# Performance work log

Measured on AMD Instinct MI355X. Metric: run time of the kernel, lower is better.

## Reference

```python
import jax, jax.numpy as jnp
import numpy as np

B, S, D = 4, 2048, 1024
H = 8  # hardcoded in AttentionLayer
HD = D // H
FF = 4096
EPS = 1e-5


def _layernorm(x):
    # LayerNorm(hidden_dim, elementwise_affine=False), eps=1e-5
    mu = jnp.mean(x, axis=-1, keepdims=True)
    var = jnp.var(x, axis=-1, keepdims=True)
    return (x - mu) / jnp.sqrt(var + EPS)


def setup_inputs() -> dict:
    key = jax.random.key(0)
    ks = jax.random.split(key, 5)
    scale = 0.02
    return {
        "x": jax.random.normal(ks[0], (B, S, D), dtype=jnp.float32),
        "qkv_proj": jax.random.normal(ks[1], (D, 3 * D), dtype=jnp.float32) * scale,
        "o_proj": jax.random.normal(ks[2], (D, D), dtype=jnp.float32) * scale,
        "ff1": jax.random.normal(ks[3], (D, FF), dtype=jnp.float32) * scale,
        "ff2": jax.random.normal(ks[4], (FF, D), dtype=jnp.float32) * scale,
    }


def reference(x, qkv_proj, o_proj, ff1, ff2):
    b, s, d = x.shape
    # --- attention ---
    qkv = jnp.matmul(x, qkv_proj)                       # [b,s,3d]
    qkv = qkv.reshape(b, s, H, 3 * HD).transpose(0, 2, 1, 3)  # [b,h,s,3hd]
    q, k, v = jnp.split(qkv, 3, axis=-1)                # each [b,h,s,hd]
    logits = jnp.einsum('bhqd,bhkd->bhqk', q, k) / jnp.sqrt(jnp.float32(HD))
    attn = jax.nn.softmax(logits, axis=-1)
    vals = jnp.einsum('bhqk,bhkd->bhqd', attn, v)       # [b,h,s,hd]
    vals = vals.transpose(0, 2, 1, 3).reshape(b, s, d)
    attn_out = jnp.matmul(vals, o_proj)
    # --- residual + norm + FFN + residual + norm ---
    x = _layernorm(x + attn_out)
    ff_out = jnp.matmul(jax.nn.relu(jnp.matmul(x, ff1)), ff2)
    x = _layernorm(x + ff_out)
    return x
```

## Files before the change

kernel.cpp:

```cpp
#include <hip/hip_runtime.h>
#include <hip/hip_bf16.h>


typedef float floatx4 __attribute__((ext_vector_type(4)));
typedef float floatx16 __attribute__((ext_vector_type(16)));
typedef short bf16x8 __attribute__((ext_vector_type(8)));

#define DEVI __device__ __forceinline__

typedef const __attribute__((address_space(1))) unsigned int* gas1_t;
typedef __attribute__((address_space(3))) unsigned int* las3_t;

DEVI void gll16(const void* g, void* l) {
  __builtin_amdgcn_global_load_lds((gas1_t)g, (las3_t)l, 16, 0, 0);
}

DEVI short bfbits(float f) {
  __hip_bfloat16 h = __float2bfloat16(f);
  return *reinterpret_cast<short*>(&h);
}

template<int EPI>
__global__ __launch_bounds__(256) void gemm_bt(
    const __hip_bfloat16* __restrict__ A,
    const __hip_bfloat16* __restrict__ BT,
    float* __restrict__ Cf, __hip_bfloat16* __restrict__ Cb,
    const float* __restrict__ Rf, const __hip_bfloat16* __restrict__ Rb,
    int M, int N, int K)
{
  __shared__ __hip_bfloat16 As[128 * 32];
  __shared__ __hip_bfloat16 Bs[128 * 32];
  const int tid = threadIdx.x;
  const int wave = tid >> 6, lane = tid & 63;
  const int lane15 = lane & 15, quad = lane >> 4;
  const int row0 = blockIdx.x * 128, col0 = blockIdx.y * 128;
  const int wr = (wave >> 1) * 64, wc = (wave & 1) * 64;

  floatx4 acc[4][4] = {};

  const int swg = ((tid & 3) ^ ((tid >> 2) & 3)) * 8;
  const __hip_bfloat16* Ag = A + (size_t)(row0 + (tid >> 2)) * K + swg;
  const __hip_bfloat16* Bg = BT + (size_t)(col0 + (tid >> 2)) * K + swg;
  char* Asl = (char*)As + tid * 16;
  char* Bsl = (char*)Bs + tid * 16;
  const size_t rstep = (size_t)64 * K;

  for (int k0 = 0; k0 < K; k0 += 32) {
    __syncthreads();
    gll16(Ag + k0, Asl);
    gll16(Ag + k0 + rstep, Asl + 4096);
    gll16(Bg + k0, Bsl);
    gll16(Bg + k0 + rstep, Bsl + 4096);
    __syncthreads();
    bf16x8 af[4], bb[4];
#pragma unroll
    for (int t = 0; t < 4; t++) {
      const int r = wr + t * 16 + lane15;
      af[t] = *(const bf16x8*)((const char*)As + (size_t)(r * 4 + (quad ^ (lane15 & 3))) * 16);
    }
#pragma unroll
    for (int t = 0; t < 4; t++) {
      const int r = wc + t * 16 + lane15;
      bb[t] = *(const bf16x8*)((const char*)Bs + (size_t)(r * 4 + (quad ^ (lane15 & 3))) * 16);
    }
#pragma unroll
    for (int i = 0; i < 4; i++)
#pragma unroll
      for (int j = 0; j < 4; j++)
        acc[i][j] = __builtin_amdgcn_mfma_f32_16x16x32_bf16(af[i], bb[j], acc[i][j], 0, 0, 0);
  }

#pragma unroll
  for (int i = 0; i < 4; i++) {
    const int mb = row0 + wr + i * 16 + quad * 4;
#pragma unroll
    for (int j = 0; j < 4; j++) {
      const int n = col0 + wc + j * 16 + lane15;
#pragma unroll
      for (int r = 0; r < 4; r++) {
        const size_t idx = (size_t)(mb + r) * N + n;
        const float v = acc[i][j][r];
        if (EPI == 0) {
          Cb[idx] = __float2bfloat16(v);
        } else if (EPI == 1) {
          Cf[idx] = v + Rf[idx];
        } else if (EPI == 2) {
          Cb[idx] = __float2bfloat16(v > 0.f ? v : 0.f);
        } else {
          Cf[idx] = v + __bfloat162float(Rb[idx]);
        }
      }
    }
  }
}

__global__ __launch_bounds__(256, 2) void attn_kernel(
    const __hip_bfloat16* __restrict__ qkv,
    const __hip_bfloat16* __restrict__ Vt,
    __hip_bfloat16* __restrict__ vals)
{
  __shared__ __hip_bfloat16 KVs[128 * 128];
  __shared__ __hip_bfloat16 QP[128 * 128];

  const int tid = threadIdx.x;
  const int wave = tid >> 6, lane = tid & 63;
  const int l31 = lane & 31, l5 = lane >> 5;
  const int qt = blockIdx.x, bh = blockIdx.y;
  const int b = bh >> 3, h = bh & 7;
  const size_t tokbase = (size_t)b * 2048;
  const float scale = 0.08838834764831845f;

  const int sw8 = ((tid & 15) ^ (tid >> 4)) * 8;
  const int srow = tid >> 4;
  const __hip_bfloat16* qg  = qkv + (tokbase + qt * 128) * 3072 + h * 384 + sw8;
  const __hip_bfloat16* kg0 = qkv + tokbase * 3072 + h * 384 + 128 + sw8;
  const __hip_bfloat16* vg0 = Vt + (size_t)bh * 128 * 2048 + sw8;

#pragma unroll
  for (int rd = 0; rd < 8; rd++)
    gll16(qg + (size_t)(rd * 16 + srow) * 3072, (char*)QP + rd * 4096 + tid * 16);
  __syncthreads();

  const int rx = l31 & 15;
  bf16x8 qf[8];
  {
    const char* qb = (const char*)QP + (wave * 32 + l31) * 256;
#pragma unroll
    for (int ks = 0; ks < 8; ks++)
      qf[ks] = *(const bf16x8*)(qb + (((ks * 2 + l5) ^ rx) << 4));
  }

  floatx16 oacc[4] = {};
  float lsum[16];
#pragma unroll
  for (int r = 0; r < 16; r++) lsum[r] = 0.f;

  for (int kt = 0; kt < 16; kt++) {
    __syncthreads();
#pragma unroll
    for (int rd = 0; rd < 8; rd++)
      gll16(kg0 + (size_t)(kt * 128 + rd * 16 + srow) * 3072,
            (char*)KVs + rd * 4096 + tid * 16);
    __syncthreads();

    floatx16 sacc[4] = {};
#pragma unroll
    for (int ks = 0; ks < 8; ks++) {
      const char* kb = (const char*)KVs + l31 * 256 + (((ks * 2 + l5) ^ rx) << 4);
#pragma unroll
      for (int nt = 0; nt < 4; nt++) {
        const bf16x8 bk = *(const bf16x8*)(kb + nt * 8192);
        sacc[nt] = __builtin_amdgcn_mfma_f32_32x32x16_bf16(qf[ks], bk, sacc[nt], 0, 0, 0);
      }
    }

    const int pbase = wave * 8192 + l5 * 1024 + (l31 & 7) * 2;
#pragma unroll
    for (int g = 0; g < 4; g++) {
      const int hgx = l5 + 2 * (g & 1);
#pragma unroll
      for (int r3 = 0; r3 < 4; r3++) {
        const int r = g * 4 + r3;
        const int rowoff = (r3 << 8) + (g << 11) + ((((l31 >> 3) ^ r3)) << 4);
        float part = 0.f;
#pragma unroll
        for (int t = 0; t < 4; t++) {
          const float p = __expf(sacc[t][r] * scale);
          part += p;
          *(short*)((char*)QP + pbase + rowoff + ((t ^ hgx) << 6)) = bfbits(p);
        }
        lsum[r] += part;
      }
    }

    __syncthreads();
#pragma unroll
    for (int rd = 0; rd < 8; rd++)
      gll16(vg0 + (size_t)kt * 128 + (size_t)(rd * 16 + srow) * 2048,
            (char*)KVs + rd * 4096 + tid * 16);
    __syncthreads();

#pragma unroll
    for (int ks = 0; ks < 8; ks++) {
      const bf16x8 ap = *(const bf16x8*)((const char*)QP +
          (wave * 32 + l31) * 256 + (((ks * 2 + l5) ^ rx) << 4));
      const char* vb = (const char*)KVs + l31 * 256 + (((ks * 2 + l5) ^ rx) << 4);
#pragma unroll
      for (int nt = 0; nt < 4; nt++) {
        const bf16x8 bv = *(const bf16x8*)(vb + nt * 8192);
        oacc[nt] = __builtin_amdgcn_mfma_f32_32x32x16_bf16(ap, bv, oacc[nt], 0, 0, 0);
      }
    }
  }

#pragma unroll
  for (int r = 0; r < 16; r++) {
#pragma unroll
    for (int off = 1; off < 32; off <<= 1)
      lsum[r] += __shfl_xor(lsum[r], off);
  }

  const size_t orow0 = tokbase + (size_t)qt * 128 + wave * 32;
#pragma unroll
  for (int g = 0; g < 4; g++) {
#pragma unroll
    for (int r3 = 0; r3 < 4; r3++) {
      const int r = g * 4 + r3;
      const float linv = 1.f / lsum[r];
      const size_t row = orow0 + r3 + 8 * g + 4 * l5;
#pragma unroll
      for (int nt = 0; nt < 4; nt++)
        vals[row * 1024 + h * 128 + nt * 32 + l31] =
            __float2bfloat16(oacc[nt][r] * linv);
    }
  }
}

__global__ __launch_bounds__(256) void cvt_bf16_k(const float* __restrict__ in,
                                                  __hip_bfloat16* __restrict__ out) {
  const size_t i = (size_t)blockIdx.x * 256 + threadIdx.x;
  const float4 v = ((const float4*)in)[i];
  short4 sv;
  sv.x = bfbits(v.x); sv.y = bfbits(v.y); sv.z = bfbits(v.z); sv.w = bfbits(v.w);
  ((short4*)out)[i] = sv;
}

__global__ __launch_bounds__(256) void wtrans_k(const float* __restrict__ W,
                                                __hip_bfloat16* __restrict__ WT,
                                                int K, int N) {
  __shared__ float t[32][33];
  const int tx = threadIdx.x & 31, ty = threadIdx.x >> 5;
  const int n0 = blockIdx.x * 32, k0 = blockIdx.y * 32;
#pragma unroll
  for (int i = 0; i < 4; i++)
    t[ty + i * 8][tx] = W[(size_t)(k0 + ty + i * 8) * N + n0 + tx];
  __syncthreads();
#pragma unroll
  for (int i = 0; i < 4; i++)
    WT[(size_t)(n0 + ty + i * 8) * K + k0 + tx] = __float2bfloat16(t[tx][ty + i * 8]);
}

__global__ __launch_bounds__(256) void vtrans_k(const __hip_bfloat16* __restrict__ qkv,
                                                __hip_bfloat16* __restrict__ Vt) {
  __shared__ __hip_bfloat16 t[32][33];
  const int tx = threadIdx.x & 31, ty = threadIdx.x >> 5;
  const int s0 = blockIdx.x * 32, d0 = blockIdx.y * 32, bh = blockIdx.z;
  const int b = bh >> 3, h = bh & 7;
#pragma unroll
  for (int i = 0; i < 4; i++)
    t[ty + i * 8][tx] = qkv[((size_t)b * 2048 + s0 + ty + i * 8) * 3072 + h * 384 + 256 + d0 + tx];
  __syncthreads();
#pragma unroll
  for (int i = 0; i < 4; i++)
    Vt[((size_t)bh * 128 + d0 + ty + i * 8) * 2048 + s0 + tx] = t[tx][ty + i * 8];
}

template<bool FINAL>
__global__ __launch_bounds__(256) void ln_k(const float* __restrict__ y,
                                            __hip_bfloat16* __restrict__ ob,
                                            float* __restrict__ of) {
  const int row = blockIdx.x, tid = threadIdx.x;
  const float4 v = ((const float4*)(y + (size_t)row * 1024))[tid];
  float s = v.x + v.y + v.z + v.w;
  float q = v.x * v.x + v.y * v.y + v.z * v.z + v.w * v.w;
#pragma unroll
  for (int off = 32; off; off >>= 1) { s += __shfl_xor(s, off); q += __shfl_xor(q, off); }
  __shared__ float ss[4], sq[4];
  const int wave = tid >> 6;
  if ((tid & 63) == 0) { ss[wave] = s; sq[wave] = q; }
  __syncthreads();
  s = ss[0] + ss[1] + ss[2] + ss[3];
  q = sq[0] + sq[1] + sq[2] + sq[3];
  const float mean = s * (1.f / 1024.f);
  const float var = q * (1.f / 1024.f) - mean * mean;
  const float rstd = rsqrtf(var + 1e-5f);
  float4 o;
  o.x = (v.x - mean) * rstd; o.y = (v.y - mean) * rstd;
  o.z = (v.z - mean) * rstd; o.w = (v.w - mean) * rstd;
  if (FINAL) {
    ((float4*)(of + (size_t)row * 1024))[tid] = o;
  } else {
    short4 sv;
    sv.x = bfbits(o.x); sv.y = bfbits(o.y); sv.z = bfbits(o.z); sv.w = bfbits(o.w);
    ((short4*)(ob + (size_t)row * 1024))[tid] = sv;
  }
}

extern "C" void kernel_launch(void* const* d_in, const int* in_sizes, int n_in,
                              void* d_out, int out_size, void* d_ws, size_t ws_size,
                              hipStream_t stream) {
  const float* x    = (const float*)d_in[0];
  const float* qkvw = (const float*)d_in[1];
  const float* ow   = (const float*)d_in[2];
  const float* f1   = (const float*)d_in[3];
  const float* f2   = (const float*)d_in[4];
  float* out = (float*)d_out;

  char* ws = (char*)d_ws;
  const size_t MB = 1024 * 1024;
  __hip_bfloat16* xb   = (__hip_bfloat16*)(ws);
  __hip_bfloat16* vals = xb;
  __hip_bfloat16* qkvT = (__hip_bfloat16*)(ws + 16 * MB);
  __hip_bfloat16* oT   = (__hip_bfloat16*)(ws + 22 * MB);
  __hip_bfloat16* f1T  = (__hip_bfloat16*)(ws + 24 * MB);
  __hip_bfloat16* f2T  = (__hip_bfloat16*)(ws + 32 * MB);
  __hip_bfloat16* qkvb = (__hip_bfloat16*)(ws + 40 * MB);
  __hip_bfloat16* Vt   = (__hip_bfloat16*)(ws + 88 * MB);
  __hip_bfloat16* hmid = qkvb;
  float* y1 = (float*)(ws + 104 * MB);
  float* y2 = y1;
  __hip_bfloat16* x1b = (__hip_bfloat16*)(ws + 136 * MB);
  (void)in_sizes; (void)n_in; (void)out_size; (void)ws_size;

  cvt_bf16_k<<<8192, 256, 0, stream>>>(x, xb);
  wtrans_k<<<dim3(96, 32), 256, 0, stream>>>(qkvw, qkvT, 1024, 3072);
  wtrans_k<<<dim3(32, 32), 256, 0, stream>>>(ow, oT, 1024, 1024);
  wtrans_k<<<dim3(128, 32), 256, 0, stream>>>(f1, f1T, 1024, 4096);
  wtrans_k<<<dim3(32, 128), 256, 0, stream>>>(f2, f2T, 4096, 1024);
  gemm_bt<0><<<dim3(64, 24), 256, 0, stream>>>(xb, qkvT, nullptr, qkvb,
                                               nullptr, nullptr, 8192, 3072, 1024);
  vtrans_k<<<dim3(64, 4, 32), 256, 0, stream>>>(qkvb, Vt);
  attn_kernel<<<dim3(16, 32), 256, 0, stream>>>(qkvb, Vt, vals);
  gemm_bt<1><<<dim3(64, 8), 256, 0, stream>>>(vals, oT, y1, nullptr,
                                              x, nullptr, 8192, 1024, 1024);
  ln_k<false><<<8192, 256, 0, stream>>>(y1, x1b, nullptr);
  gemm_bt<2><<<dim3(64, 32), 256, 0, stream>>>(x1b, f1T, nullptr, hmid,
                                               nullptr, nullptr, 8192, 4096, 1024);
  gemm_bt<3><<<dim3(64, 8), 256, 0, stream>>>(hmid, f2T, y2, nullptr,
                                              nullptr, x1b, 8192, 1024, 4096);
  ln_k<true><<<8192, 256, 0, stream>>>(y2, nullptr, out);
}
```

Before: 538.3 us.

## Deepen GEMM K-tile to 64, add split-K for N=1024 GEMMs, fuse reduction into layernorm

The GEMM now stages 64-wide K tiles with an 8-way XOR swizzle, which halves the number of barrier pairs per K loop. It also sets launch bounds to 4 waves-per-EU occupancy. The two N=1024 GEMMs (o_proj and ff2) run as 2-way split-K over a z grid dimension so they launch twice as many blocks and fill the device better. Their partial sums go to separate fp32 buffers, and the layernorm kernel now adds both partials and the residual before normalizing. This costs extra fp32 partial-buffer traffic and doubles the shared memory per block.

```diff
diff --git a/kernel.cpp b/kernel.cpp
--- a/kernel.cpp
+++ b/kernel.cpp
@@ -20,56 +20,65 @@
   return *reinterpret_cast<short*>(&h);
 }
 
-template<int EPI>
-__global__ __launch_bounds__(256) void gemm_bt(
+template<int EPI, int SPLITK>
+__global__ __launch_bounds__(256, 4) void gemm_bt(
     const __hip_bfloat16* __restrict__ A,
     const __hip_bfloat16* __restrict__ BT,
-    float* __restrict__ Cf, __hip_bfloat16* __restrict__ Cb,
-    const float* __restrict__ Rf, const __hip_bfloat16* __restrict__ Rb,
+    float* __restrict__ Cf, float* __restrict__ Cf2,
+    __hip_bfloat16* __restrict__ Cb,
     int M, int N, int K)
 {
-  __shared__ __hip_bfloat16 As[128 * 32];
-  __shared__ __hip_bfloat16 Bs[128 * 32];
+  __shared__ __hip_bfloat16 As[128 * 64];
+  __shared__ __hip_bfloat16 Bs[128 * 64];
   const int tid = threadIdx.x;
   const int wave = tid >> 6, lane = tid & 63;
   const int lane15 = lane & 15, quad = lane >> 4;
   const int row0 = blockIdx.x * 128, col0 = blockIdx.y * 128;
   const int wr = (wave >> 1) * 64, wc = (wave & 1) * 64;
+  const int Kh = K / SPLITK;
+  const size_t kofs = (SPLITK > 1) ? (size_t)blockIdx.z * Kh : 0;
 
   floatx4 acc[4][4] = {};
 
-  const int swg = ((tid & 3) ^ ((tid >> 2) & 3)) * 8;
-  const __hip_bfloat16* Ag = A + (size_t)(row0 + (tid >> 2)) * K + swg;
-  const __hip_bfloat16* Bg = BT + (size_t)(col0 + (tid >> 2)) * K + swg;
+  const int srow = tid >> 3;
+  const int sblk = (tid & 7) ^ (srow & 7);
+  const __hip_bfloat16* Ag = A + (size_t)(row0 + srow) * K + kofs + sblk * 8;
+  const __hip_bfloat16* Bg = BT + (size_t)(col0 + srow) * K + kofs + sblk * 8;
   char* Asl = (char*)As + tid * 16;
   char* Bsl = (char*)Bs + tid * 16;
-  const size_t rstep = (size_t)64 * K;
-
-  for (int k0 = 0; k0 < K; k0 += 32) {
-    __syncthreads();
-    gll16(Ag + k0, Asl);
-    gll16(Ag + k0 + rstep, Asl + 4096);
-    gll16(Bg + k0, Bsl);
-    gll16(Bg + k0 + rstep, Bsl + 4096);
-    __syncthreads();
-    bf16x8 af[4], bb[4];
-#pragma unroll
-    for (int t = 0; t < 4; t++) {
-      const int r = wr + t * 16 + lane15;
-      af[t] = *(const bf16x8*)((const char*)As + (size_t)(r * 4 + (quad ^ (lane15 & 3))) * 16);
-    }
-#pragma unroll
-    for (int t = 0; t < 4; t++) {
-      const int r = wc + t * 16 + lane15;
-      bb[t] = *(const bf16x8*)((const char*)Bs + (size_t)(r * 4 + (quad ^ (lane15 & 3))) * 16);
-    }
-#pragma unroll
-    for (int i = 0; i < 4; i++)
-#pragma unroll
-      for (int j = 0; j < 4; j++)
-        acc[i][j] = __builtin_amdgcn_mfma_f32_16x16x32_bf16(af[i], bb[j], acc[i][j], 0, 0, 0);
-  }
-
+  const size_t rstep = (size_t)32 * K;
+
+  const int x7 = lane15 & 7;
+  for (int k0 = 0; k0 < Kh; k0 += 64) {
+    __syncthreads();
+#pragma unroll
+    for (int p = 0; p < 4; p++) {
+      gll16(Ag + k0 + p * rstep, Asl + p * 4096);
+      gll16(Bg + k0 + p * rstep, Bsl + p * 4096);
+    }
+    __syncthreads();
+#pragma unroll
+    for (int kc = 0; kc < 2; kc++) {
+      bf16x8 af[4], bb[4];
+#pragma unroll
+      for (int t = 0; t < 4; t++) {
+        const int r = wr + t * 16 + lane15;
+        af[t] = *(const bf16x8*)((const char*)As + r * 128 + (((kc * 4 + quad) ^ x7) << 4));
+      }
+#pragma unroll
+      for (int t = 0; t < 4; t++) {
+        const int r = wc + t * 16 + lane15;
+        bb[t] = *(const bf16x8*)((const char*)Bs + r * 128 + (((kc * 4 + quad) ^ x7) << 4));
+      }
+#pragma unroll
+      for (int i = 0; i < 4; i++)
+#pragma unroll
+        for (int j = 0; j < 4; j++)
+          acc[i][j] = __builtin_amdgcn_mfma_f32_16x16x32_bf16(af[i], bb[j], acc[i][j], 0, 0, 0);
+    }
+  }
+
+  float* Cp = (SPLITK > 1 && blockIdx.z) ? Cf2 : Cf;
 #pragma unroll
   for (int i = 0; i < 4; i++) {
     const int mb = row0 + wr + i * 16 + quad * 4;
@@ -82,12 +91,10 @@
         const float v = acc[i][j][r];
         if (EPI == 0) {
           Cb[idx] = __float2bfloat16(v);
-        } else if (EPI == 1) {
-          Cf[idx] = v + Rf[idx];
         } else if (EPI == 2) {
           Cb[idx] = __float2bfloat16(v > 0.f ? v : 0.f);
         } else {
-          Cf[idx] = v + __bfloat162float(Rb[idx]);
+          Cp[idx] = v;
         }
       }
     }
@@ -255,12 +262,27 @@
     Vt[((size_t)bh * 128 + d0 + ty + i * 8) * 2048 + s0 + tx] = t[tx][ty + i * 8];
 }
 
-template<bool FINAL>
-__global__ __launch_bounds__(256) void ln_k(const float* __restrict__ y,
-                                            __hip_bfloat16* __restrict__ ob,
-                                            float* __restrict__ of) {
+template<bool RES_BF16, bool FINAL>
+__global__ __launch_bounds__(256) void ln_red_k(
+    const float* __restrict__ p0, const float* __restrict__ p1,
+    const float* __restrict__ resf, const __hip_bfloat16* __restrict__ resb,
+    __hip_bfloat16* __restrict__ ob, float* __restrict__ of) {
   const int row = blockIdx.x, tid = threadIdx.x;
-  const float4 v = ((const float4*)(y + (size_t)row * 1024))[tid];
+  const size_t base = (size_t)row * 1024;
+  const float4 a = ((const float4*)(p0 + base))[tid];
+  const float4 bb = ((const float4*)(p1 + base))[tid];
+  float4 v;
+  if (RES_BF16) {
+    const short4 rb = ((const short4*)(resb + base))[tid];
+    v.x = a.x + bb.x + __bfloat162float(*(const __hip_bfloat16*)&rb.x);
+    v.y = a.y + bb.y + __bfloat162float(*(const __hip_bfloat16*)&rb.y);
+    v.z = a.z + bb.z + __bfloat162float(*(const __hip_bfloat16*)&rb.z);
+    v.w = a.w + bb.w + __bfloat162float(*(const __hip_bfloat16*)&rb.w);
+  } else {
+    const float4 rf = ((const float4*)(resf + base))[tid];
+    v.x = a.x + bb.x + rf.x; v.y = a.y + bb.y + rf.y;
+    v.z = a.z + bb.z + rf.z; v.w = a.w + bb.w + rf.w;
+  }
   float s = v.x + v.y + v.z + v.w;
   float q = v.x * v.x + v.y * v.y + v.z * v.z + v.w * v.w;
 #pragma unroll
@@ -278,11 +300,11 @@
   o.x = (v.x - mean) * rstd; o.y = (v.y - mean) * rstd;
   o.z = (v.z - mean) * rstd; o.w = (v.w - mean) * rstd;
   if (FINAL) {
-    ((float4*)(of + (size_t)row * 1024))[tid] = o;
+    ((float4*)(of + base))[tid] = o;
   } else {
     short4 sv;
     sv.x = bfbits(o.x); sv.y = bfbits(o.y); sv.z = bfbits(o.z); sv.w = bfbits(o.w);
-    ((short4*)(ob + (size_t)row * 1024))[tid] = sv;
+    ((short4*)(ob + base))[tid] = sv;
   }
 }
 
@@ -300,16 +322,18 @@
   const size_t MB = 1024 * 1024;
   __hip_bfloat16* xb   = (__hip_bfloat16*)(ws);
   __hip_bfloat16* vals = xb;
+  float*          P1f  = (float*)(ws);
   __hip_bfloat16* qkvT = (__hip_bfloat16*)(ws + 16 * MB);
   __hip_bfloat16* oT   = (__hip_bfloat16*)(ws + 22 * MB);
   __hip_bfloat16* f1T  = (__hip_bfloat16*)(ws + 24 * MB);
   __hip_bfloat16* f2T  = (__hip_bfloat16*)(ws + 32 * MB);
   __hip_bfloat16* qkvb = (__hip_bfloat16*)(ws + 40 * MB);
   __hip_bfloat16* Vt   = (__hip_bfloat16*)(ws + 88 * MB);
-  __hip_bfloat16* hmid = qkvb;
-  float* y1 = (float*)(ws + 104 * MB);
-  float* y2 = y1;
-  __hip_bfloat16* x1b = (__hip_bfloat16*)(ws + 136 * MB);
+  float*          P0o  = (float*)(ws + 40 * MB);
+  float*          P1o  = (float*)(ws + 72 * MB);
+  __hip_bfloat16* hmid = (__hip_bfloat16*)(ws + 40 * MB);
+  float*          P0f  = (float*)(ws + 104 * MB);
+  __hip_bfloat16* x1b  = (__hip_bfloat16*)(ws + 136 * MB);
   (void)in_sizes; (void)n_in; (void)out_size; (void)ws_size;
 
   cvt_bf16_k<<<8192, 256, 0, stream>>>(x, xb);
@@ -317,16 +341,16 @@
   wtrans_k<<<dim3(32, 32), 256, 0, stream>>>(ow, oT, 1024, 1024);
   wtrans_k<<<dim3(128, 32), 256, 0, stream>>>(f1, f1T, 1024, 4096);
   wtrans_k<<<dim3(32, 128), 256, 0, stream>>>(f2, f2T, 4096, 1024);
-  gemm_bt<0><<<dim3(64, 24), 256, 0, stream>>>(xb, qkvT, nullptr, qkvb,
-                                               nullptr, nullptr, 8192, 3072, 1024);
+  gemm_bt<0, 1><<<dim3(64, 24, 1), 256, 0, stream>>>(xb, qkvT, nullptr, nullptr,
+                                                     qkvb, 8192, 3072, 1024);
   vtrans_k<<<dim3(64, 4, 32), 256, 0, stream>>>(qkvb, Vt);
   attn_kernel<<<dim3(16, 32), 256, 0, stream>>>(qkvb, Vt, vals);
-  gemm_bt<1><<<dim3(64, 8), 256, 0, stream>>>(vals, oT, y1, nullptr,
-                                              x, nullptr, 8192, 1024, 1024);
-  ln_k<false><<<8192, 256, 0, stream>>>(y1, x1b, nullptr);
-  gemm_bt<2><<<dim3(64, 32), 256, 0, stream>>>(x1b, f1T, nullptr, hmid,
-                                               nullptr, nullptr, 8192, 4096, 1024);
-  gemm_bt<3><<<dim3(64, 8), 256, 0, stream>>>(hmid, f2T, y2, nullptr,
-                                              nullptr, x1b, 8192, 1024, 4096);
-  ln_k<true><<<8192, 256, 0, stream>>>(y2, nullptr, out);
-}
+  gemm_bt<4, 2><<<dim3(64, 8, 2), 256, 0, stream>>>(vals, oT, P0o, P1o,
+                                                    nullptr, 8192, 1024, 1024);
+  ln_red_k<false, false><<<8192, 256, 0, stream>>>(P0o, P1o, x, nullptr, x1b, nullptr);
+  gemm_bt<2, 1><<<dim3(64, 32, 1), 256, 0, stream>>>(x1b, f1T, nullptr, nullptr,
+                                                     hmid, 8192, 4096, 1024);
+  gemm_bt<4, 2><<<dim3(64, 8, 2), 256, 0, stream>>>(hmid, f2T, P0f, P1f,
+                                                    nullptr, 8192, 1024, 4096);
+  ln_red_k<true, true><<<8192, 256, 0, stream>>>(P0f, P1f, nullptr, x1b, nullptr, out);
+}
```

Measured after the change: 490.0 us. 1.1x faster.
